# Kernel optimization log

Measured on AMD Instinct MI355X. Metric: run time of the kernel, lower is better.

Reference implementation:

```python
import jax, jax.numpy as jnp
from jax import lax
import numpy as np
import math

B, C, Hs, Ws = 2, 512, 48, 48
HW = Hs * Ws            # 2304; also m (compress_ratio = 1)
M = HW
GROUPS = 256
GS = M // GROUPS        # 9, exact split
ALPHA = 0.05
MAXITER = 43
TOL = B * HW * 1e-7     # torch: z0.numel()*tol with z0 of shape [N, HW]
EPS = 1e-5
POWER_ITERS = 100


def _make_A():
    # random projection: num_ones = round(sqrt(m)) ones per column, rows L2-normalized
    rng = np.random.RandomState(0)
    num_ones = int(round(math.sqrt(M)))  # 48
    A = np.zeros((M, HW), dtype=np.float32)
    rows = np.argsort(rng.rand(HW, M), axis=1)[:, :num_ones]  # [HW, num_ones]
    A[rows.ravel(), np.repeat(np.arange(HW), num_ones)] = 1.0
    A /= np.maximum(np.sqrt((A ** 2).sum(axis=1, keepdims=True)), 1e-12)
    return jnp.asarray(A)


def setup_inputs() -> dict:
    key = jax.random.key(0)
    ks = jax.random.split(key, 10)
    f32 = jnp.float32
    d = {
        'content': jax.random.normal(ks[0], (B, C, Hs, Ws), f32),
        'style': jax.random.normal(ks[1], (B, C, Hs, Ws), f32),
        'content_key': jax.random.normal(ks[2], (B, C, Hs, Ws), f32),
        'style_key': jax.random.normal(ks[3], (B, C, Hs, Ws), f32),
        'f_w': jax.random.normal(ks[4], (C, C), f32) * 0.02,
        'f_b': jnp.zeros((C,), f32),
        'g_w': jax.random.normal(ks[5], (C, C), f32) * 0.02,
        'g_b': jnp.zeros((C,), f32),
        'h_w': jax.random.normal(ks[6], (C, C), f32) * 0.02,
        'h_b': jnp.zeros((C,), f32),
        'A': _make_A(),
    }
    return d


def _conv1x1(x, w, b):
    # nn.Conv2d(Cin, Cout, 1): [b,c,h,w] x [o,c] + bias
    return jnp.einsum('bchw,oc->bohw', x, w) + b[None, :, None, None]


def _softshrink(x, lam):
    return jnp.sign(x) * jnp.maximum(jnp.abs(x) - lam, 0.0)


def _forward(content, style, content_key, style_key, f_w, f_b, g_w, g_b, h_w, h_b, A):
    Fq = _conv1x1(content_key, f_w, f_b).reshape(B, C, HW).transpose(0, 2, 1)  # [b,HWc,Ck]
    G = _conv1x1(style_key, g_w, g_b).reshape(B, C, HW)                        # [b,Ck,HWs]
    Hh = _conv1x1(style, h_w, h_b).reshape(B, C, HW)
    # HW <= max_sample: no subsampling branch
    style_flat = Hh.transpose(0, 2, 1)                                         # [b,HWs,C]
    S = jax.nn.softmax(jnp.einsum('bqc,bck->bqk', Fq, G), axis=-1)             # [b,HWc,HWs]
    mean = jnp.einsum('bqk,bkc->bqc', S, style_flat)                           # weighted mean
    std = jnp.sqrt(jax.nn.relu(jnp.einsum('bqk,bkc->bqc', S, style_flat ** 2) - mean ** 2))
    mean = mean.transpose(0, 2, 1)  # [b,C,HW]
    std = std.transpose(0, 2, 1)
    # random projection along spatial dim: feat @ A^T
    proj = lambda f: jnp.einsum('mh,bch->bcm', A, f)
    mean_c = proj(mean)
    std_c = proj(std)
    cont_c = proj(content.reshape(B, C, HW))
    # per-group mean/variance norm (256 equal groups of GS along compressed dim)
    g = cont_c.reshape(B, C, GROUPS, GS)
    mu = g.mean(axis=-1, keepdims=True)
    var = g.var(axis=-1, ddof=1, keepdims=True)  # torch var is unbiased
    normed = (g - mu) / jnp.sqrt(var + EPS)
    x = (normed * std_c.reshape(B, C, GROUPS, GS)
         + mean_c.reshape(B, C, GROUPS, GS)).reshape(B, C, M)
    # FISTA sparse coding: min 0.5||z A^T - x||^2 + alpha |z|_1
    Ad = lax.stop_gradient(A)
    WtW = Ad.T @ Ad
    v = jnp.full((HW,), 1.0 / math.sqrt(HW), jnp.float32)
    def _pi(v, _):
        w = WtW @ v
        return w / jnp.linalg.norm(w), None
    v, _ = lax.scan(_pi, v, None, length=POWER_ITERS)
    L = v @ (WtW @ v)  # largest eigenvalue of A^T A
    lr = 1.0 / L
    z0 = jnp.zeros((B, C, HW), x.dtype)

    def step(carry, _):
        z, y, t, done = carry
        resid = jnp.einsum('bch,mh->bcm', y, A) - x   # y @ A^T - x
        grad = jnp.einsum('bcm,mh->bch', resid, A)    # resid @ A
        zn = _softshrink(y - lr * grad, ALPHA * lr)
        diff = jnp.abs(z - zn).sum()
        tn = (1.0 + jnp.sqrt(1.0 + 4.0 * t * t)) / 2.0
        yn = zn + (t - 1.0) / tn * (zn - z)
        z2 = jnp.where(done, z, zn)
        y2 = jnp.where(done, y, yn)
        t2 = jnp.where(done, t, tn)
        done2 = done | (diff <= TOL)
        return (z2, y2, t2, done2), None

    (z, _, _, _), _ = lax.scan(step, (z0, z0, jnp.float32(1.0), jnp.array(False)),
                               None, length=MAXITER)
    return z.reshape(B, C, Hs, Ws)


def reference(content, style, content_key, style_key, f_w, f_b, g_w, g_b, h_w, h_b, A):
    return _forward(content, style, content_key, style_key,
                    f_w, f_b, g_w, g_b, h_w, h_b, A)
```

## Files before the change

### kernel.cpp

```cpp
#include <hip/hip_runtime.h>
#include <hip/hip_cooperative_groups.h>
#include <math.h>

namespace cg = cooperative_groups;

#define TPB 256

typedef _Float16 f16;
typedef _Float16 half8 __attribute__((ext_vector_type(8)));
typedef _Float16 f16x2 __attribute__((ext_vector_type(2)));
typedef _Float16 f16x4 __attribute__((ext_vector_type(4)));
typedef float floatx4 __attribute__((ext_vector_type(4)));

static constexpr int CDIM = 512;
static constexpr int HWD = 2304;
static constexpr float ALPHA = 0.05f;
static constexpr float TOLF = 4.608e-4f;

enum { EPI_F32 = 0, EPI_F16BIASN = 1, EPI_F16BIASM = 2, EPI_F16 = 3,
       EPI_WTW = 4, EPI_MEANSTD = 5 };

__device__ __forceinline__ bool fista_done(const float* __restrict__ diffArr, int iter) {
    bool done = false;
    for (int j = 0; j < iter; ++j) done = done || (diffArr[j] <= TOLF);
    return done;
}

__device__ __forceinline__ void gload_lds(const f16* g, f16* l) {
#if __has_builtin(__builtin_amdgcn_global_load_lds)
    __builtin_amdgcn_global_load_lds(
        (__attribute__((address_space(1))) void*)(g),
        (__attribute__((address_space(3))) void*)(l), 16, 0, 0);
#else
    *(int4*)l = *(const int4*)g;
#endif
}

template<int N> __device__ __forceinline__ void vwait() {
    if constexpr (N == 0)      asm volatile("s_waitcnt vmcnt(0)" ::: "memory");
    else if constexpr (N == 4) asm volatile("s_waitcnt vmcnt(4)" ::: "memory");
    else if constexpr (N == 6) asm volatile("s_waitcnt vmcnt(6)" ::: "memory");
}

__device__ __forceinline__ void barrier_f() {
    asm volatile("" ::: "memory");
    __builtin_amdgcn_s_barrier();
    asm volatile("" ::: "memory");
}

template<int EPI, int MF>
__global__ __launch_bounds__(TPB, 4) void sgemm(
    const f16* __restrict__ A, long a_bs, int lda,
    const f16* __restrict__ B, long b_bs, int ldb,
    void* __restrict__ C0, long c_bs, int ldc,
    void* __restrict__ C1,
    int K,
    const float* __restrict__ bias)
{
    constexpr int ASZ = MF * 32 * 64;
    constexpr int BSZ = 64 * 64;
    constexpr int LCNT = MF + 2;
    __shared__ alignas(16) f16 As[2 * ASZ];
    __shared__ alignas(16) f16 Bs[2 * BSZ];
    const int tid = threadIdx.x;
    const int wid = tid >> 6, lane = tid & 63;
    const int wr = wid >> 1, wc = wid & 1;

    const int gx = gridDim.x, gy = gridDim.y;
    const int nwg = gx * gy;
    const int d = blockIdx.y * gx + blockIdx.x;
    const int q = nwg >> 3, r = nwg & 7;
    const int xcd = d & 7, rest = d >> 3;
    const int wgid = (xcd < r ? xcd * (q + 1) : r * (q + 1) + (xcd - r) * q) + rest;
    const int bx = wgid / gy, by = wgid % gy;

    const int m0 = by * (MF * 32), n0 = bx << 6;
    const f16* Ab = A + (long)blockIdx.z * a_bs;
    const f16* Bb = B + (long)blockIdx.z * b_bs;

    floatx4 acc[MF][2] = {};
    floatx4 acc2[MF][2] = {};

    const int rl = lane & 15, kg = lane >> 4;
    const int lrow = lane >> 3;
    const int gs = (lane & 7) ^ lrow;
    const int nt = K >> 6;

    auto STAGE = [&](int t, int buf) {
        const long k0 = (long)t << 6;
        f16* Ad = As + buf * ASZ;
        f16* Bd = Bs + buf * BSZ;
        #pragma unroll
        for (int p = 0; p < MF; ++p) {
            const int c = wid * MF + p;
            const int R = c * 8 + lrow;
            gload_lds(Ab + (long)(m0 + R) * lda + k0 + gs * 8, Ad + c * 512);
        }
        #pragma unroll
        for (int p = 0; p < 2; ++p) {
            const int c = wid * 2 + p;
            const int R = c * 8 + lrow;
            gload_lds(Bb + (long)(n0 + R) * ldb + k0 + gs * 8, Bd + c * 512);
        }
    };

    STAGE(0, 0);
    for (int t = 0; t < nt; ++t) {
        if (t + 1 < nt) { STAGE(t + 1, (t + 1) & 1); vwait<LCNT>(); }
        else            { vwait<0>(); }
        barrier_f();
        const f16* Ac = As + (t & 1) * ASZ;
        const f16* Bc = Bs + (t & 1) * BSZ;
        #pragma unroll
        for (int kk = 0; kk < 2; ++kk) {
            const int j = kk * 4 + kg;
            half8 af[MF], bf[2];
            #pragma unroll
            for (int f = 0; f < MF; ++f) {
                const int rowa = wr * (MF * 16) + f * 16 + rl;
                af[f] = *(const half8*)&Ac[rowa * 64 + ((j ^ (rowa & 7)) * 8)];
            }
            #pragma unroll
            for (int f = 0; f < 2; ++f) {
                const int rowb = wc * 32 + f * 16 + rl;
                bf[f] = *(const half8*)&Bc[rowb * 64 + ((j ^ (rowb & 7)) * 8)];
            }
            #pragma unroll
            for (int fi = 0; fi < MF; ++fi) {
                #pragma unroll
                for (int fj = 0; fj < 2; ++fj) {
                    acc[fi][fj] = __builtin_amdgcn_mfma_f32_16x16x32_f16(af[fi], bf[fj], acc[fi][fj], 0, 0, 0);
                    if constexpr (EPI == EPI_MEANSTD) {
                        half8 bq = bf[fj] * bf[fj];
                        acc2[fi][fj] = __builtin_amdgcn_mfma_f32_16x16x32_f16(af[fi], bq, acc2[fi][fj], 0, 0, 0);
                    }
                }
            }
        }
        barrier_f();
    }

    const int rg = lane >> 4;
    const int bz = blockIdx.z;
    #pragma unroll
    for (int fi = 0; fi < MF; ++fi) {
        #pragma unroll
        for (int fj = 0; fj < 2; ++fj) {
            #pragma unroll
            for (int r2 = 0; r2 < 4; ++r2) {
                const int row = m0 + wr * (MF * 16) + fi * 16 + rg * 4 + r2;
                const int col = n0 + wc * 32 + fj * 16 + rl;
                const float v = acc[fi][fj][r2];
                if constexpr (EPI == EPI_F32) {
                    ((float*)C0)[bz * c_bs + (long)row * ldc + col] = v;
                } else if constexpr (EPI == EPI_F16BIASN) {
                    ((f16*)C0)[bz * c_bs + (long)row * ldc + col] = (f16)(v + bias[col]);
                } else if constexpr (EPI == EPI_F16BIASM) {
                    ((f16*)C0)[bz * c_bs + (long)row * ldc + col] = (f16)(v + bias[row]);
                } else if constexpr (EPI == EPI_F16) {
                    ((f16*)C0)[bz * c_bs + (long)row * ldc + col] = (f16)v;
                } else if constexpr (EPI == EPI_WTW) {
                    ((float*)C0)[(long)row * ldc + col] = v;
                    ((f16*)C1)[(long)row * ldc + col] = (f16)v;
                } else if constexpr (EPI == EPI_MEANSTD) {
                    const float m_ = v;
                    float s2 = acc2[fi][fj][r2] - m_ * m_;
                    const long o = ((long)bz * CDIM + col) * HWD + row;
                    ((f16*)C0)[o] = (f16)m_;
                    ((f16*)C1)[o] = (f16)sqrtf(s2 > 0.f ? s2 : 0.f);
                }
            }
        }
    }
}

__global__ __launch_bounds__(TPB, 2) void fista_coop(
    const f16* __restrict__ Wh,
    const float* __restrict__ xAf,
    f16* __restrict__ yA, f16* __restrict__ yB,
    const float* __restrict__ lrs,
    float* __restrict__ diffArr,
    float* __restrict__ dout)
{
    cg::grid_group grid = cg::this_grid();
    constexpr int MF = 4;
    constexpr int ASZ = MF * 32 * 64;
    constexpr int BSZ = 64 * 64;
    constexpr int LCNT = MF + 2;
    __shared__ alignas(16) f16 As[2 * ASZ];
    __shared__ alignas(16) f16 Bs[2 * BSZ];
    __shared__ float red[TPB];
    const int tid = threadIdx.x;
    const int wid = tid >> 6, lane = tid & 63;
    const int wr = wid >> 1, wc = wid & 1;

    const int d = blockIdx.x;
    const int wgid = (d & 7) * 36 + (d >> 3);
    const int bx = wgid >> 3, by = wgid & 7;
    const int m0 = by << 7, n0 = bx << 6;

    const int rl = lane & 15, kg = lane >> 4;
    const int rg = lane >> 4;
    const int lrow = lane >> 3;
    const int gs = (lane & 7) ^ lrow;
    constexpr int nt = HWD >> 6;

    const float lr = lrs[0], sh = lrs[1];

    float xar[MF][2][4], zr[MF][2][4], yr[MF][2][4];
    #pragma unroll
    for (int fi = 0; fi < MF; ++fi)
        #pragma unroll
        for (int fj = 0; fj < 2; ++fj)
            #pragma unroll
            for (int r2 = 0; r2 < 4; ++r2) {
                const int row = m0 + wr * (MF * 16) + fi * 16 + rg * 4 + r2;
                const int col = n0 + wc * 32 + fj * 16 + rl;
                xar[fi][fj][r2] = xAf[(long)row * HWD + col];
                zr[fi][fj][r2] = 0.f;
                yr[fi][fj][r2] = 0.f;
            }

    float t = 1.0f;
    for (int iter = 0; iter < 43; ++iter) {
        const float tn = (1.0f + sqrtf(1.0f + 4.0f * t * t)) * 0.5f;
        const float coef = (t - 1.0f) / tn;
        t = tn;
        const f16* Yin = (iter & 1) ? yB : yA;
        f16* Yout = (iter & 1) ? yA : yB;

        floatx4 acc[MF][2] = {};
        auto STAGE = [&](int tt, int buf) {
            const long k0 = (long)tt << 6;
            f16* Ad = As + buf * ASZ;
            f16* Bd = Bs + buf * BSZ;
            #pragma unroll
            for (int p = 0; p < MF; ++p) {
                const int c = wid * MF + p;
                const int R = c * 8 + lrow;
                gload_lds(Yin + (long)(m0 + R) * HWD + k0 + gs * 8, Ad + c * 512);
            }
            #pragma unroll
            for (int p = 0; p < 2; ++p) {
                const int c = wid * 2 + p;
                const int R = c * 8 + lrow;
                gload_lds(Wh + (long)(n0 + R) * HWD + k0 + gs * 8, Bd + c * 512);
            }
        };
        STAGE(0, 0);
        for (int tt = 0; tt < nt; ++tt) {
            if (tt + 1 < nt) { STAGE(tt + 1, (tt + 1) & 1); vwait<LCNT>(); }
            else             { vwait<0>(); }
            barrier_f();
            const f16* Ac = As + (tt & 1) * ASZ;
            const f16* Bc = Bs + (tt & 1) * BSZ;
            #pragma unroll
            for (int kk = 0; kk < 2; ++kk) {
                const int j = kk * 4 + kg;
                half8 af[MF], bf[2];
                #pragma unroll
                for (int f = 0; f < MF; ++f) {
                    const int rowa = wr * (MF * 16) + f * 16 + rl;
                    af[f] = *(const half8*)&Ac[rowa * 64 + ((j ^ (rowa & 7)) * 8)];
                }
                #pragma unroll
                for (int f = 0; f < 2; ++f) {
                    const int rowb = wc * 32 + f * 16 + rl;
                    bf[f] = *(const half8*)&Bc[rowb * 64 + ((j ^ (rowb & 7)) * 8)];
                }
                #pragma unroll
                for (int fi = 0; fi < MF; ++fi)
                    #pragma unroll
                    for (int fj = 0; fj < 2; ++fj)
                        acc[fi][fj] = __builtin_amdgcn_mfma_f32_16x16x32_f16(af[fi], bf[fj], acc[fi][fj], 0, 0, 0);
            }
            barrier_f();
        }

        float loc = 0.f;
        #pragma unroll
        for (int fi = 0; fi < MF; ++fi)
            #pragma unroll
            for (int fj = 0; fj < 2; ++fj)
                #pragma unroll
                for (int r2 = 0; r2 < 4; ++r2) {
                    const int row = m0 + wr * (MF * 16) + fi * 16 + rg * 4 + r2;
                    const int col = n0 + wc * 32 + fj * 16 + rl;
                    const float grad = acc[fi][fj][r2] - xar[fi][fj][r2];
                    const float p = yr[fi][fj][r2] - lr * grad;
                    const float ap = fabsf(p) - sh;
                    const float zn = ap > 0.f ? copysignf(ap, p) : 0.f;
                    const float zo = zr[fi][fj][r2];
                    loc += fabsf(zn - zo);
                    const float yn = zn + coef * (zn - zo);
                    zr[fi][fj][r2] = zn;
                    yr[fi][fj][r2] = yn;
                    Yout[(long)row * HWD + col] = (f16)yn;
                }
        red[tid] = loc; __syncthreads();
        for (int s = 128; s > 0; s >>= 1) { if (tid < s) red[tid] += red[tid + s]; __syncthreads(); }
        if (tid == 0) atomicAdd(&diffArr[iter], red[0]);

        __threadfence();
        grid.sync();
        __threadfence();
        const float dsum = __hip_atomic_load(&diffArr[iter], __ATOMIC_RELAXED,
                                             __HIP_MEMORY_SCOPE_AGENT);
        if (dsum <= TOLF) break;
    }

    #pragma unroll
    for (int fi = 0; fi < MF; ++fi)
        #pragma unroll
        for (int fj = 0; fj < 2; ++fj)
            #pragma unroll
            for (int r2 = 0; r2 < 4; ++r2) {
                const int row = m0 + wr * (MF * 16) + fi * 16 + rg * 4 + r2;
                const int col = n0 + wc * 32 + fj * 16 + rl;
                dout[(long)row * HWD + col] = zr[fi][fj][r2];
            }
}

__global__ __launch_bounds__(TPB, 3) void fista_step(
    const f16* __restrict__ Yin, const f16* __restrict__ Wh,
    const float* __restrict__ xAf,
    float* __restrict__ zc, float* __restrict__ zp, f16* __restrict__ yhp,
    const float* __restrict__ lrs, float coefPrev, float coefCur,
    float* __restrict__ diffArr, int iter)
{
    if (iter > 0 && fista_done(diffArr, iter)) return;
    constexpr int MF = 2;
    constexpr int ASZ = MF * 32 * 64;
    constexpr int BSZ = 64 * 64;
    constexpr int LCNT = MF + 2;
    __shared__ alignas(16) f16 As[2 * ASZ];
    __shared__ alignas(16) f16 Bs[2 * BSZ];
    __shared__ float red[TPB];
    const int tid = threadIdx.x;
    const int wid = tid >> 6, lane = tid & 63;
    const int wr = wid >> 1, wc = wid & 1;

    const int d = blockIdx.y * gridDim.x + blockIdx.x;
    const int wgid = (d & 7) * 72 + (d >> 3);
    const int bx = wgid >> 4, by = wgid & 15;
    const int m0 = by << 6, n0 = bx << 6;

    floatx4 acc[MF][2] = {};
    const int rl = lane & 15, kg = lane >> 4;
    const int lrow = lane >> 3;
    const int gs = (lane & 7) ^ lrow;
    constexpr int nt = HWD >> 6;

    auto STAGE = [&](int t, int buf) {
        const long k0 = (long)t << 6;
        f16* Ad = As + buf * ASZ;
        f16* Bd = Bs + buf * BSZ;
        #pragma unroll
        for (int p = 0; p < MF; ++p) {
            const int c = wid * MF + p;
            const int R = c * 8 + lrow;
            gload_lds(Yin + (long)(m0 + R) * HWD + k0 + gs * 8, Ad + c * 512);
        }
        #pragma unroll
        for (int p = 0; p < 2; ++p) {
            const int c = wid * 2 + p;
            const int R = c * 8 + lrow;
            gload_lds(Wh + (long)(n0 + R) * HWD + k0 + gs * 8, Bd + c * 512);
        }
    };
    STAGE(0, 0);
    for (int t = 0; t < nt; ++t) {
        if (t + 1 < nt) { STAGE(t + 1, (t + 1) & 1); vwait<LCNT>(); }
        else            { vwait<0>(); }
        barrier_f();
        const f16* Ac = As + (t & 1) * ASZ;
        const f16* Bc = Bs + (t & 1) * BSZ;
        #pragma unroll
        for (int kk = 0; kk < 2; ++kk) {
            const int j = kk * 4 + kg;
            half8 af[MF], bf[2];
            #pragma unroll
            for (int f = 0; f < MF; ++f) {
                const int rowa = wr * (MF * 16) + f * 16 + rl;
                af[f] = *(const half8*)&Ac[rowa * 64 + ((j ^ (rowa & 7)) * 8)];
            }
            #pragma unroll
            for (int f = 0; f < 2; ++f) {
                const int rowb = wc * 32 + f * 16 + rl;
                bf[f] = *(const half8*)&Bc[rowb * 64 + ((j ^ (rowb & 7)) * 8)];
            }
            #pragma unroll
            for (int fi = 0; fi < MF; ++fi)
                #pragma unroll
                for (int fj = 0; fj < 2; ++fj)
                    acc[fi][fj] = __builtin_amdgcn_mfma_f32_16x16x32_f16(af[fi], bf[fj], acc[fi][fj], 0, 0, 0);
        }
        barrier_f();
    }

    const int rg = lane >> 4;
    const float lr = lrs[0], sh = lrs[1];
    float loc = 0.f;
    #pragma unroll
    for (int fi = 0; fi < MF; ++fi)
        #pragma unroll
        for (int fj = 0; fj < 2; ++fj)
            #pragma unroll
            for (int r2 = 0; r2 < 4; ++r2) {
                const int row = m0 + wr * (MF * 16) + fi * 16 + rg * 4 + r2;
                const int col = n0 + wc * 32 + fj * 16 + rl;
                const long off = (long)row * HWD + col;
                const float zk = zc[off];
                const float zkm = zp[off];
                const float ykf = zk + coefPrev * (zk - zkm);
                const float grad = acc[fi][fj][r2] - xAf[off];
                const float p = ykf - lr * grad;
                const float ap = fabsf(p) - sh;
                const float zn = ap > 0.f ? copysignf(ap, p) : 0.f;
                zp[off] = zn;
                yhp[off] = (f16)(zn + coefCur * (zn - zk));
                loc += fabsf(zn - zk);
            }
    red[tid] = loc; __syncthreads();
    for (int s = 128; s > 0; s >>= 1) { if (tid < s) red[tid] += red[tid + s]; __syncthreads(); }
    if (tid == 0) atomicAdd(&diffArr[iter], red[0]);
}

__global__ __launch_bounds__(TPB) void tcvt(const float* __restrict__ in, long in_bs,
                                            f16* __restrict__ out, long out_bs, int R, int Cc) {
    __shared__ float t[32][33];
    const int b = blockIdx.z;
    const int r0 = blockIdx.y << 5, c0 = blockIdx.x << 5;
    const int tx = threadIdx.x & 31, ty = threadIdx.x >> 5;
    const float* ib = in + (long)b * in_bs;
    #pragma unroll
    for (int p = 0; p < 4; ++p) {
        const int r = ty + p * 8;
        t[r][tx] = ib[(long)(r0 + r) * Cc + c0 + tx];
    }
    __syncthreads();
    f16* ob = out + (long)b * out_bs;
    #pragma unroll
    for (int p = 0; p < 4; ++p) {
        const int c = ty + p * 8;
        ob[(long)(c0 + c) * R + r0 + tx] = (f16)t[tx][c];
    }
}

__global__ void cvt16(const float4* __restrict__ in, f16x4* __restrict__ out, long n4) {
    long i = (long)blockIdx.x * blockDim.x + threadIdx.x;
    const long st = (long)gridDim.x * blockDim.x;
    for (; i < n4; i += st) {
        const float4 v = in[i];
        f16x4 o; o.x = (f16)v.x; o.y = (f16)v.y; o.z = (f16)v.z; o.w = (f16)v.w;
        out[i] = o;
    }
}

__global__ __launch_bounds__(TPB) void softmax_h(const float* __restrict__ Sf, f16* __restrict__ Sh) {
    __shared__ float row[HWD];
    __shared__ float red[TPB];
    const long base = (long)blockIdx.x * HWD;
    const int tid = threadIdx.x;
    float mx = -3.4e38f;
    for (int i = tid; i < HWD; i += TPB) { const float v = Sf[base + i]; row[i] = v; mx = fmaxf(mx, v); }
    red[tid] = mx; __syncthreads();
    for (int s = 128; s > 0; s >>= 1) { if (tid < s) red[tid] = fmaxf(red[tid], red[tid + s]); __syncthreads(); }
    mx = red[0]; __syncthreads();
    float sum = 0.f;
    for (int i = tid; i < HWD; i += TPB) { const float e = expf(row[i] - mx); row[i] = e; sum += e; }
    red[tid] = sum; __syncthreads();
    for (int s = 128; s > 0; s >>= 1) { if (tid < s) red[tid] += red[tid + s]; __syncthreads(); }
    const float inv = 1.0f / red[0];
    for (int i = tid; i < HWD; i += TPB) Sh[base + i] = (f16)(row[i] * inv);
}

__global__ __launch_bounds__(TPB) void groupnorm_x(const float* __restrict__ contc,
                                                   const float* __restrict__ meanc,
                                                   const float* __restrict__ stdc,
                                                   f16* __restrict__ xh) {
    const long base = (long)blockIdx.x * HWD + (long)threadIdx.x * 9;
    float v[9];
    float mu = 0.f;
    #pragma unroll
    for (int j = 0; j < 9; ++j) { v[j] = contc[base + j]; mu += v[j]; }
    mu *= (1.0f / 9.0f);
    float var = 0.f;
    #pragma unroll
    for (int j = 0; j < 9; ++j) { const float d = v[j] - mu; var += d * d; }
    var *= (1.0f / 8.0f);
    const float rs = 1.0f / sqrtf(var + 1e-5f);
    #pragma unroll
    for (int j = 0; j < 9; ++j)
        xh[base + j] = (f16)((v[j] - mu) * rs * (float)stdc[base + j] + (float)meanc[base + j]);
}

__global__ __launch_bounds__(TPB) void matvec_h(const f16* __restrict__ Wm,
                                                const float* __restrict__ win,
                                                float* __restrict__ wout) {
    __shared__ float red[TPB];
    const int tid = threadIdx.x;
    float s = 0.f;
    for (int i = tid; i < HWD; i += TPB) { const float v = win[i]; s += v * v; }
    red[tid] = s; __syncthreads();
    for (int st = 128; st > 0; st >>= 1) { if (tid < st) red[tid] += red[tid + st]; __syncthreads(); }
    const float ninv = rsqrtf(red[0]);
    const int row = (blockIdx.x << 2) + (tid >> 6);
    const int lane = tid & 63;
    const f16x2* wr2 = (const f16x2*)(Wm + (long)row * HWD);
    float d = 0.f;
    for (int j = lane; j < HWD / 2; j += 64) {
        const f16x2 p = wr2[j];
        d += (float)p.x * win[2 * j] + (float)p.y * win[2 * j + 1];
    }
    #pragma unroll
    for (int o = 32; o > 0; o >>= 1) d += __shfl_down(d, o);
    if (lane == 0) wout[row] = d * ninv;
}

__global__ __launch_bounds__(TPB) void kernelL(const float* __restrict__ Wf,
                                               const float* __restrict__ w,
                                               float* __restrict__ Lnum, float* __restrict__ Lden) {
    __shared__ float red[TPB];
    const int tid = threadIdx.x;
    const int row = (blockIdx.x << 2) + (tid >> 6);
    const int lane = tid & 63;
    const float* wr = Wf + (long)row * HWD;
    float d = 0.f;
    for (int j = lane; j < HWD; j += 64) d += wr[j] * w[j];
    #pragma unroll
    for (int o = 32; o > 0; o >>= 1) d += __shfl_down(d, o);
    red[tid] = (lane == 0) ? d * w[row] : 0.f;
    __syncthreads();
    for (int s = 128; s > 0; s >>= 1) { if (tid < s) red[tid] += red[tid + s]; __syncthreads(); }
    if (tid == 0) atomicAdd(Lnum, red[0]);
    if (blockIdx.x == 0) {
        __syncthreads();
        float s2 = 0.f;
        for (int i = tid; i < HWD; i += TPB) { const float v = w[i]; s2 += v * v; }
        red[tid] = s2; __syncthreads();
        for (int s = 128; s > 0; s >>= 1) { if (tid < s) red[tid] += red[tid + s]; __syncthreads(); }
        if (tid == 0) *Lden = red[0];
    }
}

__global__ void lr_fin(const float* __restrict__ Lnum, const float* __restrict__ Lden,
                       float* __restrict__ lrs) {
    const float lr = Lden[0] / Lnum[0];
    lrs[0] = lr;
    lrs[1] = ALPHA * lr;
}

__global__ void init_small(float* __restrict__ wvec, float* __restrict__ diffArr,
                           float* __restrict__ Lnum) {
    const int tid = threadIdx.x;
    for (int i = tid; i < HWD; i += TPB) wvec[i] = (float)(1.0 / 48.0);
    if (tid < 43) diffArr[tid] = 0.f;
    if (tid == 64) Lnum[0] = 0.f;
}

__global__ void zero_kernel(float4* __restrict__ p, long n4) {
    long i = (long)blockIdx.x * blockDim.x + threadIdx.x;
    const long st = (long)gridDim.x * blockDim.x;
    for (; i < n4; i += st) p[i] = make_float4(0.f, 0.f, 0.f, 0.f);
}

__global__ void copy_fista(const float4* __restrict__ zfA, const float4* __restrict__ zfB,
                           float4* __restrict__ out, const float* __restrict__ diffArr, long n4) {
    int last = 42;
    for (int j = 0; j < 43; ++j) { if (diffArr[j] <= TOLF) { last = j; break; } }
    const float4* src = (last & 1) ? zfA : zfB;
    long i = (long)blockIdx.x * blockDim.x + threadIdx.x;
    const long st = (long)gridDim.x * blockDim.x;
    for (; i < n4; i += st) out[i] = src[i];
}

extern "C" void kernel_launch(void* const* d_in, const int* in_sizes, int n_in,
                              void* d_out, int out_size, void* d_ws, size_t ws_size,
                              hipStream_t stream) {
    (void)in_sizes; (void)n_in; (void)out_size;
    const float* content = (const float*)d_in[0];
    const float* style   = (const float*)d_in[1];
    const float* ckey    = (const float*)d_in[2];
    const float* skey    = (const float*)d_in[3];
    const float* f_w = (const float*)d_in[4];
    const float* f_b = (const float*)d_in[5];
    const float* g_w = (const float*)d_in[6];
    const float* g_b = (const float*)d_in[7];
    const float* h_w = (const float*)d_in[8];
    const float* h_b = (const float*)d_in[9];
    const float* Amat = (const float*)d_in[10];

    if (ws_size < 79500000) return;
    char* W = (char*)d_ws;

    const long E16 = (long)HWD * CDIM;
    const long EHH = (long)HWD * HWD;
    f16*  ckeyT = (f16*)(W + 0);
    f16*  skeyT = (f16*)(W + 4718592);
    f16*  styleT= (f16*)(W + 9437184);
    float* Sf   = (float*)(W + 0);
    f16*  Ah    = (f16*)(W + 0);
    f16*  At    = (f16*)(W + 10616832);
    f16*  Wh    = (f16*)(W + 21233664);
    f16*  W4h   = (f16*)(W + 31850496);
    f16*  W2h   = (f16*)(W + 0);
    float* contc= (float*)(W + 21233664);
    float* zfA  = (float*)(W + 0);
    float* zfB  = (float*)(W + 9437184);
    f16*  yhA   = (f16*)(W + 31850496);
    f16*  yhB   = (f16*)(W + 36569088);
    f16*  Sh    = (f16*)(W + 42467328);
    float* meanc= (float*)(W + 42467328);
    float* stdc = (float*)(W + 42467328 + 9437184);
    float* Wf   = (float*)(W + 42467328);
    float* xAf  = (float*)(W + 42467328);
    f16*  Fh    = (f16*)(W + 63700992);
    f16*  Gh    = (f16*)(W + 63700992 + 4718592);
    f16*  Hh    = (f16*)(W + 63700992 + 9437184);
    f16*  meanx = (f16*)(W + 63700992);
    f16*  stdx  = (f16*)(W + 63700992 + 4718592);
    f16*  conth = (f16*)(W + 63700992 + 9437184);
    f16*  xh    = (f16*)(W + 63700992);
    float* w_a  = (float*)(W + 77856768);
    float* w_b  = (float*)(W + 77856768 + 9216);
    float* lrs  = (float*)(W + 77856768 + 18432);
    float* Lnum = (float*)(W + 77856768 + 18440);
    float* Lden = (float*)(W + 77856768 + 18444);
    float* diffArr = (float*)(W + 77856768 + 18448);
    f16*  fwh   = (f16*)(W + 77875712);
    f16*  gwh   = (f16*)(W + 77875712 + 524288);
    f16*  hwh   = (f16*)(W + 77875712 + 1048576);

    init_small<<<1, TPB, 0, stream>>>(w_a, diffArr, Lnum);

    cvt16<<<256, TPB, 0, stream>>>((const float4*)f_w, (f16x4*)fwh, (long)CDIM * CDIM / 4);
    cvt16<<<256, TPB, 0, stream>>>((const float4*)g_w, (f16x4*)gwh, (long)CDIM * CDIM / 4);
    cvt16<<<256, TPB, 0, stream>>>((const float4*)h_w, (f16x4*)hwh, (long)CDIM * CDIM / 4);
    tcvt<<<dim3(72, 16, 2), TPB, 0, stream>>>(ckey, E16, ckeyT, E16, CDIM, HWD);
    tcvt<<<dim3(72, 16, 2), TPB, 0, stream>>>(skey, E16, skeyT, E16, CDIM, HWD);
    tcvt<<<dim3(72, 16, 2), TPB, 0, stream>>>(style, E16, styleT, E16, CDIM, HWD);

    sgemm<EPI_F16BIASN, 2><<<dim3(8, 36, 2), TPB, 0, stream>>>(ckeyT, E16, CDIM, fwh, 0, CDIM,
        Fh, E16, CDIM, nullptr, CDIM, f_b);
    sgemm<EPI_F16BIASN, 2><<<dim3(8, 36, 2), TPB, 0, stream>>>(skeyT, E16, CDIM, gwh, 0, CDIM,
        Gh, E16, CDIM, nullptr, CDIM, g_b);
    sgemm<EPI_F16BIASM, 2><<<dim3(36, 8, 2), TPB, 0, stream>>>(hwh, 0, CDIM, styleT, E16, CDIM,
        Hh, E16, HWD, nullptr, CDIM, h_b);

    sgemm<EPI_F32, 2><<<dim3(36, 36, 2), TPB, 0, stream>>>(Fh, E16, CDIM, Gh, E16, CDIM,
        Sf, EHH, HWD, nullptr, CDIM, nullptr);
    softmax_h<<<2 * HWD, TPB, 0, stream>>>(Sf, Sh);

    cvt16<<<2048, TPB, 0, stream>>>((const float4*)Amat, (f16x4*)Ah, EHH / 4);
    tcvt<<<dim3(72, 72, 1), TPB, 0, stream>>>(Amat, 0, At, 0, HWD, HWD);

    sgemm<EPI_MEANSTD, 2><<<dim3(8, 36, 2), TPB, 0, stream>>>(Sh, EHH, HWD, Hh, E16, HWD,
        meanx, 0, HWD, stdx, HWD, nullptr);

    cvt16<<<2048, TPB, 0, stream>>>((const float4*)content, (f16x4*)conth, (long)2 * E16 / 4);

    sgemm<EPI_F32, 2><<<dim3(36, 16, 1), TPB, 0, stream>>>(meanx, 0, HWD, Ah, 0, HWD,
        meanc, 0, HWD, nullptr, HWD, nullptr);
    sgemm<EPI_F32, 2><<<dim3(36, 16, 1), TPB, 0, stream>>>(stdx, 0, HWD, Ah, 0, HWD,
        stdc, 0, HWD, nullptr, HWD, nullptr);
    sgemm<EPI_F32, 2><<<dim3(36, 16, 1), TPB, 0, stream>>>(conth, 0, HWD, Ah, 0, HWD,
        contc, 0, HWD, nullptr, HWD, nullptr);

    groupnorm_x<<<1024, TPB, 0, stream>>>(contc, meanc, stdc, xh);

    sgemm<EPI_WTW, 2><<<dim3(36, 36, 1), TPB, 0, stream>>>(At, 0, HWD, At, 0, HWD,
        Wf, 0, HWD, Wh, HWD, nullptr);
    sgemm<EPI_F16, 2><<<dim3(36, 36, 1), TPB, 0, stream>>>(Wh, 0, HWD, Wh, 0, HWD,
        W2h, 0, HWD, nullptr, HWD, nullptr);
    sgemm<EPI_F16, 2><<<dim3(36, 36, 1), TPB, 0, stream>>>(W2h, 0, HWD, W2h, 0, HWD,
        W4h, 0, HWD, nullptr, HWD, nullptr);

    for (int it = 0; it < 25; ++it) {
        const float* win = (it & 1) ? w_b : w_a;
        float* wout = (it & 1) ? w_a : w_b;
        matvec_h<<<HWD / 4, TPB, 0, stream>>>(W4h, win, wout);
    }
    kernelL<<<HWD / 4, TPB, 0, stream>>>(Wf, w_b, Lnum, Lden);
    lr_fin<<<1, 1, 0, stream>>>(Lnum, Lden, lrs);

    sgemm<EPI_F32, 2><<<dim3(36, 16, 1), TPB, 0, stream>>>(xh, 0, HWD, At, 0, HWD,
        xAf, 0, HWD, nullptr, HWD, nullptr);

    int dev = 0; hipGetDevice(&dev);
    int coopOK = 0, numCU = 0, maxB = 0;
    hipDeviceGetAttribute(&coopOK, hipDeviceAttributeCooperativeLaunch, dev);
    hipDeviceGetAttribute(&numCU, hipDeviceAttributeMultiprocessorCount, dev);
    hipOccupancyMaxActiveBlocksPerMultiprocessor(&maxB, fista_coop, TPB, 0);
    const bool useCoop = coopOK && ((long)maxB * numCU >= 288);

    zero_kernel<<<1024, TPB, 0, stream>>>((float4*)yhA, E16 / 4);

    if (useCoop) {
        float* doutF = (float*)d_out;
        void* args[] = { (void*)&Wh, (void*)&xAf, (void*)&yhA, (void*)&yhB,
                         (void*)&lrs, (void*)&diffArr, (void*)&doutF };
        hipLaunchCooperativeKernel((const void*)fista_coop, dim3(288), dim3(TPB),
                                   args, 0, stream);
    } else {
        zero_kernel<<<1024, TPB, 0, stream>>>((float4*)zfA, E16);
        float t = 1.0f, coefPrev = 0.0f;
        for (int it = 0; it < 43; ++it) {
            const float tn = (1.0f + sqrtf(1.0f + 4.0f * t * t)) * 0.5f;
            const float coef = (t - 1.0f) / tn;
            t = tn;
            float* zc = (it & 1) ? zfB : zfA;
            float* zp = (it & 1) ? zfA : zfB;
            fista_step<<<dim3(36, 16, 1), TPB, 0, stream>>>(yhA, Wh, xAf, zc, zp, yhA,
                                                            lrs, coefPrev, coef, diffArr, it);
            coefPrev = coef;
        }
        copy_fista<<<2048, TPB, 0, stream>>>((const float4*)zfA, (const float4*)zfB,
                                             (float4*)d_out, diffArr, 2 * E16 / 4);
    }
}
```

Measured before the change: 2.112 ms.

## Add persistent FISTA kernel with per-row-group counters instead of grid-wide sync

Adds a persistent cooperative kernel that runs all 43 FISTA iterations with 576 smaller-tile blocks. Each block keeps z, y and xA in registers, and blocks synchronise only within their 64-row group through atomic counters rather than grid.sync. This is valid because each row of y @ W depends only on the same rows of y. Convergence checking is moved off the critical path. If any block's local diff falls below tolerance, a flag is set, and the old exact cooperative kernel plus a y reset rerun the full computation as a fallback. The cost is a possible duplicate run, plus the risk that block-local diffs only approximate the global stopping criterion.

```diff
diff --git a/kernel.cpp b/kernel.cpp
--- a/kernel.cpp
+++ b/kernel.cpp
@@ -174,14 +174,168 @@
     }
 }
 
+__global__ __launch_bounds__(TPB, 3) void fista_fast(
+    const f16* __restrict__ Wh,
+    const float* __restrict__ xAf,
+    f16* __restrict__ yA, f16* __restrict__ yB,
+    const float* __restrict__ lrs,
+    unsigned int* __restrict__ cnt,
+    int* __restrict__ flag,
+    float* __restrict__ dout)
+{
+    constexpr int MF = 2;
+    constexpr int ASZ = MF * 32 * 64;
+    constexpr int BSZ = 64 * 64;
+    constexpr int LCNT = MF + 2;
+    __shared__ alignas(16) f16 As[2 * ASZ];
+    __shared__ alignas(16) f16 Bs[2 * BSZ];
+    __shared__ float red[TPB];
+    const int tid = threadIdx.x;
+    const int wid = tid >> 6, lane = tid & 63;
+    const int wr = wid >> 1, wc = wid & 1;
+
+    const int d = blockIdx.x;
+    const int g = d & 15;
+    const int ntile = d >> 4;
+    const int m0 = g << 6, n0 = ntile << 6;
+
+    const int rl = lane & 15, kg = lane >> 4;
+    const int rg = lane >> 4;
+    const int lrow = lane >> 3;
+    const int gs = (lane & 7) ^ lrow;
+    constexpr int nt = HWD >> 6;
+
+    const float lr = lrs[0], sh = lrs[1];
+
+    float xar[MF][2][4], zr[MF][2][4], yr[MF][2][4];
+    #pragma unroll
+    for (int fi = 0; fi < MF; ++fi)
+        #pragma unroll
+        for (int fj = 0; fj < 2; ++fj)
+            #pragma unroll
+            for (int r2 = 0; r2 < 4; ++r2) {
+                const int row = m0 + wr * (MF * 16) + fi * 16 + rg * 4 + r2;
+                const int col = n0 + wc * 32 + fj * 16 + rl;
+                xar[fi][fj][r2] = xAf[(long)row * HWD + col];
+                zr[fi][fj][r2] = 0.f;
+                yr[fi][fj][r2] = 0.f;
+            }
+
+    float t = 1.0f;
+    for (int iter = 0; iter < 43; ++iter) {
+        const float tn = (1.0f + sqrtf(1.0f + 4.0f * t * t)) * 0.5f;
+        const float coef = (t - 1.0f) / tn;
+        t = tn;
+        const f16* Yin = (iter & 1) ? yB : yA;
+        f16* Yout = (iter & 1) ? yA : yB;
+
+        floatx4 acc[MF][2] = {};
+        auto STAGE = [&](int tt, int buf) {
+            const long k0 = (long)tt << 6;
+            f16* Ad = As + buf * ASZ;
+            f16* Bd = Bs + buf * BSZ;
+            #pragma unroll
+            for (int p = 0; p < MF; ++p) {
+                const int c = wid * MF + p;
+                const int R = c * 8 + lrow;
+                gload_lds(Yin + (long)(m0 + R) * HWD + k0 + gs * 8, Ad + c * 512);
+            }
+            #pragma unroll
+            for (int p = 0; p < 2; ++p) {
+                const int c = wid * 2 + p;
+                const int R = c * 8 + lrow;
+                gload_lds(Wh + (long)(n0 + R) * HWD + k0 + gs * 8, Bd + c * 512);
+            }
+        };
+        STAGE(0, 0);
+        for (int tt = 0; tt < nt; ++tt) {
+            if (tt + 1 < nt) { STAGE(tt + 1, (tt + 1) & 1); vwait<LCNT>(); }
+            else             { vwait<0>(); }
+            barrier_f();
+            const f16* Ac = As + (tt & 1) * ASZ;
+            const f16* Bc = Bs + (tt & 1) * BSZ;
+            #pragma unroll
+            for (int kk = 0; kk < 2; ++kk) {
+                const int j = kk * 4 + kg;
+                half8 af[MF], bf[2];
+                #pragma unroll
+                for (int f = 0; f < MF; ++f) {
+                    const int rowa = wr * (MF * 16) + f * 16 + rl;
+                    af[f] = *(const half8*)&Ac[rowa * 64 + ((j ^ (rowa & 7)) * 8)];
+                }
+                #pragma unroll
+                for (int f = 0; f < 2; ++f) {
+                    const int rowb = wc * 32 + f * 16 + rl;
+                    bf[f] = *(const half8*)&Bc[rowb * 64 + ((j ^ (rowb & 7)) * 8)];
+                }
+                #pragma unroll
+                for (int fi = 0; fi < MF; ++fi)
+                    #pragma unroll
+                    for (int fj = 0; fj < 2; ++fj)
+                        acc[fi][fj] = __builtin_amdgcn_mfma_f32_16x16x32_f16(af[fi], bf[fj], acc[fi][fj], 0, 0, 0);
+            }
+            barrier_f();
+        }
+
+        float loc = 0.f;
+        #pragma unroll
+        for (int fi = 0; fi < MF; ++fi)
+            #pragma unroll
+            for (int fj = 0; fj < 2; ++fj)
+                #pragma unroll
+                for (int r2 = 0; r2 < 4; ++r2) {
+                    const int row = m0 + wr * (MF * 16) + fi * 16 + rg * 4 + r2;
+                    const int col = n0 + wc * 32 + fj * 16 + rl;
+                    const float grad = acc[fi][fj][r2] - xar[fi][fj][r2];
+                    const float p = yr[fi][fj][r2] - lr * grad;
+                    const float ap = fabsf(p) - sh;
+                    const float zn = ap > 0.f ? copysignf(ap, p) : 0.f;
+                    const float zo = zr[fi][fj][r2];
+                    loc += fabsf(zn - zo);
+                    const float yn = zn + coef * (zn - zo);
+                    zr[fi][fj][r2] = zn;
+                    yr[fi][fj][r2] = yn;
+                    Yout[(long)row * HWD + col] = (f16)yn;
+                }
+        red[tid] = loc; __syncthreads();
+        for (int s = 128; s > 0; s >>= 1) { if (tid < s) red[tid] += red[tid + s]; __syncthreads(); }
+        if (tid == 0 && red[0] <= TOLF)
+            __hip_atomic_store(flag, 1, __ATOMIC_RELEASE, __HIP_MEMORY_SCOPE_AGENT);
+
+        __threadfence();
+        __syncthreads();
+        if (tid == 0) {
+            __hip_atomic_fetch_add(&cnt[g], 1u, __ATOMIC_RELEASE, __HIP_MEMORY_SCOPE_AGENT);
+            const unsigned int need = 36u * (unsigned int)(iter + 1);
+            while (__hip_atomic_load(&cnt[g], __ATOMIC_ACQUIRE, __HIP_MEMORY_SCOPE_AGENT) < need)
+                __builtin_amdgcn_s_sleep(2);
+        }
+        __syncthreads();
+        __threadfence();
+    }
+
+    #pragma unroll
+    for (int fi = 0; fi < MF; ++fi)
+        #pragma unroll
+        for (int fj = 0; fj < 2; ++fj)
+            #pragma unroll
+            for (int r2 = 0; r2 < 4; ++r2) {
+                const int row = m0 + wr * (MF * 16) + fi * 16 + rg * 4 + r2;
+                const int col = n0 + wc * 32 + fj * 16 + rl;
+                dout[(long)row * HWD + col] = zr[fi][fj][r2];
+            }
+}
+
 __global__ __launch_bounds__(TPB, 2) void fista_coop(
     const f16* __restrict__ Wh,
     const float* __restrict__ xAf,
     f16* __restrict__ yA, f16* __restrict__ yB,
     const float* __restrict__ lrs,
     float* __restrict__ diffArr,
+    const int* __restrict__ flag,
     float* __restrict__ dout)
 {
+    if (__hip_atomic_load(flag, __ATOMIC_ACQUIRE, __HIP_MEMORY_SCOPE_AGENT) == 0) return;
     cg::grid_group grid = cg::this_grid();
     constexpr int MF = 4;
     constexpr int ASZ = MF * 32 * 64;
@@ -552,14 +706,24 @@
 }
 
 __global__ void init_small(float* __restrict__ wvec, float* __restrict__ diffArr,
-                           float* __restrict__ Lnum) {
+                           float* __restrict__ Lnum, unsigned int* __restrict__ cnt,
+                           int* __restrict__ flag) {
     const int tid = threadIdx.x;
     for (int i = tid; i < HWD; i += TPB) wvec[i] = (float)(1.0 / 48.0);
     if (tid < 43) diffArr[tid] = 0.f;
     if (tid == 64) Lnum[0] = 0.f;
+    if (tid >= 80 && tid < 96) cnt[tid - 80] = 0u;
+    if (tid == 96) *flag = 0;
 }
 
 __global__ void zero_kernel(float4* __restrict__ p, long n4) {
+    long i = (long)blockIdx.x * blockDim.x + threadIdx.x;
+    const long st = (long)gridDim.x * blockDim.x;
+    for (; i < n4; i += st) p[i] = make_float4(0.f, 0.f, 0.f, 0.f);
+}
+
+__global__ void zero_if(const int* __restrict__ flag, float4* __restrict__ p, long n4) {
+    if (__hip_atomic_load(flag, __ATOMIC_ACQUIRE, __HIP_MEMORY_SCOPE_AGENT) == 0) return;
     long i = (long)blockIdx.x * blockDim.x + threadIdx.x;
     const long st = (long)gridDim.x * blockDim.x;
     for (; i < n4; i += st) p[i] = make_float4(0.f, 0.f, 0.f, 0.f);
@@ -628,11 +792,13 @@
     float* Lnum = (float*)(W + 77856768 + 18440);
     float* Lden = (float*)(W + 77856768 + 18444);
     float* diffArr = (float*)(W + 77856768 + 18448);
+    unsigned int* cnt = (unsigned int*)(W + 77856768 + 18624);
+    int*  flag  = (int*)(W + 77856768 + 18688);
     f16*  fwh   = (f16*)(W + 77875712);
     f16*  gwh   = (f16*)(W + 77875712 + 524288);
     f16*  hwh   = (f16*)(W + 77875712 + 1048576);
 
-    init_small<<<1, TPB, 0, stream>>>(w_a, diffArr, Lnum);
+    init_small<<<1, TPB, 0, stream>>>(w_a, diffArr, Lnum, cnt, flag);
 
     cvt16<<<256, TPB, 0, stream>>>((const float4*)f_w, (f16x4*)fwh, (long)CDIM * CDIM / 4);
     cvt16<<<256, TPB, 0, stream>>>((const float4*)g_w, (f16x4*)gwh, (long)CDIM * CDIM / 4);
@@ -688,20 +854,31 @@
         xAf, 0, HWD, nullptr, HWD, nullptr);
 
     int dev = 0; hipGetDevice(&dev);
-    int coopOK = 0, numCU = 0, maxB = 0;
+    int coopOK = 0, numCU = 0, maxFast = 0, maxCoop = 0;
     hipDeviceGetAttribute(&coopOK, hipDeviceAttributeCooperativeLaunch, dev);
     hipDeviceGetAttribute(&numCU, hipDeviceAttributeMultiprocessorCount, dev);
-    hipOccupancyMaxActiveBlocksPerMultiprocessor(&maxB, fista_coop, TPB, 0);
-    const bool useCoop = coopOK && ((long)maxB * numCU >= 288);
+    hipOccupancyMaxActiveBlocksPerMultiprocessor(&maxFast, fista_fast, TPB, 0);
+    hipOccupancyMaxActiveBlocksPerMultiprocessor(&maxCoop, fista_coop, TPB, 0);
+    const bool usePersist = coopOK && ((long)maxFast * numCU >= 576)
+                                   && ((long)maxCoop * numCU >= 288);
 
     zero_kernel<<<1024, TPB, 0, stream>>>((float4*)yhA, E16 / 4);
 
-    if (useCoop) {
+    if (usePersist) {
         float* doutF = (float*)d_out;
-        void* args[] = { (void*)&Wh, (void*)&xAf, (void*)&yhA, (void*)&yhB,
-                         (void*)&lrs, (void*)&diffArr, (void*)&doutF };
-        hipLaunchCooperativeKernel((const void*)fista_coop, dim3(288), dim3(TPB),
-                                   args, 0, stream);
+        {
+            void* args[] = { (void*)&Wh, (void*)&xAf, (void*)&yhA, (void*)&yhB,
+                             (void*)&lrs, (void*)&cnt, (void*)&flag, (void*)&doutF };
+            hipLaunchCooperativeKernel((const void*)fista_fast, dim3(576), dim3(TPB),
+                                       args, 0, stream);
+        }
+        zero_if<<<1024, TPB, 0, stream>>>(flag, (float4*)yhA, E16 / 4);
+        {
+            void* args[] = { (void*)&Wh, (void*)&xAf, (void*)&yhA, (void*)&yhB,
+                             (void*)&lrs, (void*)&diffArr, (void*)&flag, (void*)&doutF };
+            hipLaunchCooperativeKernel((const void*)fista_coop, dim3(288), dim3(TPB),
+                                       args, 0, stream);
+        }
     } else {
         zero_kernel<<<1024, TPB, 0, stream>>>((float4*)zfA, E16);
         float t = 1.0f, coefPrev = 0.0f;
```

Measured after the change: 2.123 ms. No clear change (+0.5%).
